# Kernel optimization log

Measured on AMD Instinct MI355X. Metric: run time of the kernel, lower is better.

The kernel has to match this reference:

```python
import jax, jax.numpy as jnp
import numpy as np
import math

H = 16  # heads
EPS_NORM = 1e-12
EPS_W = 1e-6


def setup_inputs() -> dict:
    key = jax.random.key(0)
    ks = jax.random.split(key, 6)
    B, T, d = 2, 2048, 1024
    s = 1.0 / math.sqrt(d)
    return {
        "x": jax.random.normal(ks[0], (B, T, d), dtype=jnp.float32),
        "Wq": jax.random.normal(ks[1], (d, d), dtype=jnp.float32) * s,
        "Wk": jax.random.normal(ks[2], (d, d), dtype=jnp.float32) * s,
        "Wv": jax.random.normal(ks[3], (d, d), dtype=jnp.float32) * s,
        "Wo": jax.random.normal(ks[4], (d, d), dtype=jnp.float32) * s,
        "bo": jnp.zeros((d,), dtype=jnp.float32),
    }


def _l2norm(t):
    # F.normalize(dim=-1): x / max(||x||, eps)
    n = jnp.sqrt(jnp.sum(t * t, axis=-1, keepdims=True))
    return t / jnp.maximum(n, EPS_NORM)


def reference(x, Wq, Wk, Wv, Wo, bo):
    B, T, d = x.shape
    dk = d // H
    # projections (torch Linear: y = x @ W.T), split heads -> [B, H, T, dk]
    def proj(W):
        return (x @ W.T).reshape(B, T, H, dk).transpose(0, 2, 1, 3)
    Q = _l2norm(proj(Wq))
    K = _l2norm(proj(Wk))
    V = proj(Wv)
    # angular similarity scores [B, H, T, T]
    sim = jnp.clip(jnp.einsum("bhqd,bhkd->bhqk", Q, K), -0.999, 0.999)
    scores = 1.0 - jnp.arccos(sim) / jnp.float32(math.pi)
    W = jnp.maximum(scores, EPS_W) ** 8
    W = W / (jnp.sum(W, axis=-1, keepdims=True) + EPS_W)
    out = jnp.einsum("bhqk,bhkd->bhqd", W, V)  # [B, H, T, dk]
    out = out.transpose(0, 2, 1, 3).reshape(B, T, d)
    return out @ Wo.T + bo
```

## Files before the change

### kernel.cpp

```cpp
#include <hip/hip_runtime.h>
#include <hip/hip_bf16.h>
#include <hip/hip_fp16.h>
#include <math.h>

#define BB 2
#define TT 2048
#define DD 1024
#define HH 16
#define DK 64
#define KT 64

typedef _Float16 f16x8 __attribute__((ext_vector_type(8)));
typedef __fp16 fp16x2 __attribute__((ext_vector_type(2)));
typedef __attribute__((ext_vector_type(4))) float f32x4;
typedef __attribute__((ext_vector_type(2))) float f32x2;

static __device__ __forceinline__ void g2lds16(const void* g, void* l) {
    __builtin_amdgcn_global_load_lds(
        (const __attribute__((address_space(1))) unsigned int*)g,
        (__attribute__((address_space(3))) unsigned int*)l, 16, 0, 0);
}

static __device__ __forceinline__ f32x2 w8pair(f32x2 s, f32x2& rs) {
    f32x2 ax;
    ax.x = fminf(fabsf(s.x), 0.999f);
    ax.y = fminf(fabsf(s.y), 0.999f);
    f32x2 p = ax * -0.0059617f + 0.0236380f;
    p = p * ax + (-0.0675180f);
    p = p * ax + 0.49997851f;
    f32x2 om = 1.0f - ax;
    f32x2 u;
    u.x = __builtin_amdgcn_sqrtf(om.x);
    u.y = __builtin_amdgcn_sqrtf(om.y);
    f32x2 uq = u * p;
    f32x2 e = 0.5f - uq;
    f32x2 t;
    t.x = 0.5f + copysignf(e.x, s.x);
    t.y = 0.5f + copysignf(e.y, s.y);
    f32x2 t2 = t * t;
    f32x2 t4 = t2 * t2;
    f32x2 t8 = t4 * t4;
    rs += t8;
    return t8;
}
static __device__ __forceinline__ int packh2(f32x2 v) {
    union { fp16x2 h; int i; } u;
    u.h = __builtin_amdgcn_cvt_pkrtz(v.x, v.y);
    return u.i;
}

__global__ __launch_bounds__(256) void cvtall_kernel(
    const float* __restrict__ x,  const float* __restrict__ Wq,
    const float* __restrict__ Wk, const float* __restrict__ Wv,
    const float* __restrict__ Wo,
    _Float16* __restrict__ xh, _Float16* __restrict__ W3h,
    _Float16* __restrict__ Woh)
{
    const int bid = blockIdx.x;
    const float* s; _Float16* d; int blk;
    if (bid < 2048) { s = x; d = xh; blk = bid; }
    else {
        const int idx = bid - 2048;
        const int w   = idx >> 9;
        blk = idx & 511;
        s = (w == 0) ? Wq : (w == 1) ? Wk : (w == 2) ? Wv : Wo;
        d = (w == 3) ? Woh : W3h + (size_t)w * (DD * DD);
    }
    const int i = (blk * 256 + threadIdx.x) * 8;
    float4 a = *(const float4*)(s + i);
    float4 b = *(const float4*)(s + i + 4);
    union { _Float16 h[8]; int4 v; } u;
    u.h[0] = (_Float16)a.x; u.h[1] = (_Float16)a.y;
    u.h[2] = (_Float16)a.z; u.h[3] = (_Float16)a.w;
    u.h[4] = (_Float16)b.x; u.h[5] = (_Float16)b.y;
    u.h[6] = (_Float16)b.z; u.h[7] = (_Float16)b.w;
    *(int4*)(d + i) = u.v;
}

__global__ __launch_bounds__(256, 3) void gemm_qkv(
    const _Float16* __restrict__ Ah_g, const _Float16* __restrict__ B_g,
    _Float16* __restrict__ Qh, _Float16* __restrict__ Kh,
    _Float16* __restrict__ Vh, int nbx, int K)
{
    __shared__ _Float16 Ahs[8][128][8];
    __shared__ _Float16 Bhs[8][128][8];

    const int nwg  = gridDim.x;
    const int wgid = blockIdx.x;
    const int cpx  = nwg >> 3;
    const int swz  = (wgid & 7) * cpx + (wgid >> 3);
    const int by   = swz / nbx;
    const int bx   = swz - by * nbx;

    const int t    = threadIdx.x;
    const int m0   = by * 128;
    const int n0g  = bx * 128;
    const int seg  = n0g >> 10;
    const int n0   = n0g & 1023;

    const int lane = t & 63;
    const int w    = t >> 6;
    const int wm   = w >> 1;
    const int wn   = w & 1;
    const int l15  = lane & 15;
    const int quad = lane >> 4;

    f32x4 acc[4][4];
#pragma unroll
    for (int i = 0; i < 4; ++i)
#pragma unroll
        for (int j = 0; j < 4; ++j) acc[i][j] = (f32x4)0.f;

    for (int k0 = 0; k0 < K; k0 += 64) {
        __syncthreads();
#pragma unroll
        for (int i = 0; i < 2; ++i) {
            const int cc = w * 2 + i;
#pragma unroll
            for (int half = 0; half < 2; ++half) {
                g2lds16(Ah_g + (size_t)(m0 + half * 64 + lane) * K + k0 + cc * 8,
                        &Ahs[cc][half * 64][0]);
                g2lds16(B_g + (size_t)(n0g + half * 64 + lane) * K + k0 + cc * 8,
                        &Bhs[cc][half * 64][0]);
            }
        }
        __syncthreads();

#pragma unroll
        for (int kh = 0; kh < 2; ++kh) {
            f16x8 ah[4], bh[4];
#pragma unroll
            for (int tm = 0; tm < 4; ++tm)
                ah[tm] = *(const f16x8*)&Ahs[kh * 4 + quad][wm * 64 + tm * 16 + l15][0];
#pragma unroll
            for (int tn = 0; tn < 4; ++tn)
                bh[tn] = *(const f16x8*)&Bhs[kh * 4 + quad][wn * 64 + tn * 16 + l15][0];
#pragma unroll
            for (int tm = 0; tm < 4; ++tm)
#pragma unroll
                for (int tn = 0; tn < 4; ++tn)
                    acc[tm][tn] = __builtin_amdgcn_mfma_f32_16x16x32_f16(
                        ah[tm], bh[tn], acc[tm][tn], 0, 0, 0);
        }
    }

    if (seg < 2) {
        _Float16* __restrict__ dstb = (seg == 0) ? Qh : Kh;
        const int hh = (n0 >> 6) + wn;
#pragma unroll
        for (int tm = 0; tm < 4; ++tm) {
#pragma unroll
            for (int r = 0; r < 4; ++r) {
                float ss = 0.f;
#pragma unroll
                for (int tn = 0; tn < 4; ++tn) {
                    const float v = acc[tm][tn][r];
                    ss += v * v;
                }
                ss += __shfl_xor(ss, 1);
                ss += __shfl_xor(ss, 2);
                ss += __shfl_xor(ss, 4);
                ss += __shfl_xor(ss, 8);
                const float inv = __builtin_amdgcn_rsqf(fmaxf(ss, 1e-24f));
                const int row = m0 + wm * 64 + tm * 16 + quad * 4 + r;
                const int b   = row >> 11;
                const int tt  = row & 2047;
                _Float16* dst = dstb + ((size_t)(b * HH + hh) * TT + tt) * DK;
#pragma unroll
                for (int tn = 0; tn < 4; ++tn)
                    dst[tn * 16 + l15] = (_Float16)(acc[tm][tn][r] * inv);
            }
        }
    } else {
#pragma unroll
        for (int tm = 0; tm < 4; ++tm)
#pragma unroll
            for (int tn = 0; tn < 4; ++tn) {
                const int col  = n0 + wn * 64 + tn * 16 + l15;
                const int rowb = m0 + wm * 64 + tm * 16 + quad * 4;
#pragma unroll
                for (int r = 0; r < 4; ++r)
                    Vh[(size_t)(rowb + r) * 1024 + col] =
                        (_Float16)acc[tm][tn][r];
            }
    }
}

__global__ __launch_bounds__(256) void gemm_wo(
    const _Float16* __restrict__ Ah_g, const _Float16* __restrict__ Al_g,
    const _Float16* __restrict__ B_g, const float* __restrict__ bias,
    float* __restrict__ C, int nbx, int K)
{
    __shared__ _Float16 Ahs[2][8][128][8];
    __shared__ _Float16 Als[2][8][128][8];
    __shared__ _Float16 Bhs[2][8][128][8];

    const int nwg  = gridDim.x;
    const int wgid = blockIdx.x;
    const int cpx  = nwg >> 3;
    const int swz  = (wgid & 7) * cpx + (wgid >> 3);
    const int by   = swz / nbx;
    const int bx   = swz - by * nbx;

    const int t    = threadIdx.x;
    const int m0   = by * 128;
    const int n0g  = bx * 128;

    const int lane = t & 63;
    const int w    = t >> 6;
    const int wm   = w >> 1;
    const int wn   = w & 1;
    const int l15  = lane & 15;
    const int quad = lane >> 4;

    f32x4 acc[4][4];
#pragma unroll
    for (int i = 0; i < 4; ++i)
#pragma unroll
        for (int j = 0; j < 4; ++j) acc[i][j] = (f32x4)0.f;

    auto STAGE = [&](int bf, int k0) {
#pragma unroll
        for (int i = 0; i < 2; ++i) {
            const int cc = w * 2 + i;
#pragma unroll
            for (int half = 0; half < 2; ++half) {
                g2lds16(Ah_g + (size_t)(m0 + half * 64 + lane) * K + k0 + cc * 8,
                        &Ahs[bf][cc][half * 64][0]);
                g2lds16(Al_g + (size_t)(m0 + half * 64 + lane) * K + k0 + cc * 8,
                        &Als[bf][cc][half * 64][0]);
                g2lds16(B_g + (size_t)(n0g + half * 64 + lane) * K + k0 + cc * 8,
                        &Bhs[bf][cc][half * 64][0]);
            }
        }
    };

    STAGE(0, 0);
    int cur = 0;
    for (int k0 = 0; k0 < K; k0 += 64) {
        __syncthreads();
        if (k0 + 64 < K) STAGE(cur ^ 1, k0 + 64);

#pragma unroll
        for (int kh = 0; kh < 2; ++kh) {
            f16x8 ah[4], al[4], bh[4];
#pragma unroll
            for (int tm = 0; tm < 4; ++tm) {
                ah[tm] = *(const f16x8*)&Ahs[cur][kh * 4 + quad][wm * 64 + tm * 16 + l15][0];
                al[tm] = *(const f16x8*)&Als[cur][kh * 4 + quad][wm * 64 + tm * 16 + l15][0];
            }
#pragma unroll
            for (int tn = 0; tn < 4; ++tn)
                bh[tn] = *(const f16x8*)&Bhs[cur][kh * 4 + quad][wn * 64 + tn * 16 + l15][0];
#pragma unroll
            for (int tm = 0; tm < 4; ++tm)
#pragma unroll
                for (int tn = 0; tn < 4; ++tn)
                    acc[tm][tn] = __builtin_amdgcn_mfma_f32_16x16x32_f16(
                        ah[tm], bh[tn], acc[tm][tn], 0, 0, 0);
#pragma unroll
            for (int tm = 0; tm < 4; ++tm)
#pragma unroll
                for (int tn = 0; tn < 4; ++tn)
                    acc[tm][tn] = __builtin_amdgcn_mfma_f32_16x16x32_f16(
                        al[tm], bh[tn], acc[tm][tn], 0, 0, 0);
        }
        cur ^= 1;
    }

#pragma unroll
    for (int tm = 0; tm < 4; ++tm)
#pragma unroll
        for (int tn = 0; tn < 4; ++tn) {
            const int col  = n0g + wn * 64 + tn * 16 + l15;
            const float bv = bias[col];
            const int rowb = m0 + wm * 64 + tm * 16 + quad * 4;
#pragma unroll
            for (int r = 0; r < 4; ++r)
                C[(size_t)(rowb + r) * 1024 + col] = acc[tm][tn][r] + bv;
        }
}

__global__ __launch_bounds__(256) void vtrans_kernel(
    const _Float16* __restrict__ Vh, _Float16* __restrict__ Vt)
{
    __shared__ _Float16 Vtmp[64][72];
    const int t  = threadIdx.x;
    const int t0 = blockIdx.x * 64;
    const int h  = blockIdx.y;
    const int b  = blockIdx.z;
    const int bh = b * HH + h;

    {
        const int i  = t >> 2;
        const int jc = (t & 3) * 16;
        const _Float16* src = Vh + (size_t)(b * TT + t0 + i) * DD + h * DK + jc;
        f16x8 a = *(const f16x8*)(src);
        f16x8 c = *(const f16x8*)(src + 8);
#pragma unroll
        for (int e = 0; e < 8; ++e) {
            Vtmp[jc + e][i]     = a[e];
            Vtmp[jc + 8 + e][i] = c[e];
        }
    }
    __syncthreads();
    {
        const int d  = t >> 2;
        const int kc = (t & 3) * 16;
        const int tc = (t0 + kc) >> 3;
        _Float16* dst = Vt + ((size_t)bh * (TT >> 3) + tc) * (64 * 8) + d * 8;
        *(int4*)(dst)          = *(const int4*)&Vtmp[d][kc];
        *(int4*)(dst + 64 * 8) = *(const int4*)&Vtmp[d][kc + 8];
    }
}

__global__ __launch_bounds__(256, 4) void attn_kernel(
    const _Float16* __restrict__ Qh_g, const _Float16* __restrict__ Kh_g,
    const _Float16* __restrict__ Vt_g,
    _Float16* __restrict__ Oh, _Float16* __restrict__ Ol)
{
    __shared__ _Float16 Vts[2][8][64][8];
    __shared__ _Float16 Ws[2][64][72];
    __shared__ float Rbuf[4][64];
    __shared__ float Rfin[64];

    const int t    = threadIdx.x;
    const int lane = t & 63;
    const int w    = t >> 6;
    const int l15  = lane & 15;
    const int quad = lane >> 4;
    const int q0   = blockIdx.x * 64;
    const int h    = blockIdx.y;
    const int b    = blockIdx.z;
    const size_t bh = (size_t)(b * HH + h);

    const _Float16* kh_g = Kh_g + bh * TT * DK;
    const _Float16* vt_g = Vt_g + bh * (size_t)(TT >> 3) * (64 * 8);

    f16x8 qf[4][2];
#pragma unroll
    for (int qt = 0; qt < 4; ++qt)
#pragma unroll
        for (int s = 0; s < 2; ++s)
            qf[qt][s] = *(const f16x8*)(Qh_g + (bh * TT + q0 + qt * 16 + l15) * DK
                                        + s * 32 + quad * 8);

    f16x8 kf[2], kfn[2];
#pragma unroll
    for (int s = 0; s < 2; ++s) {
        kf[s] = *(const f16x8*)(kh_g
            + (size_t)(w * 16 + l15) * DK + s * 32 + quad * 8);
        kfn[s] = kf[s];
    }

#pragma unroll
    for (int j = 0; j < 2; ++j) {
        const int kc = w * 2 + j;
        g2lds16(vt_g + (size_t)kc * (64 * 8) + lane * 8, &Vts[0][kc][0][0]);
    }

    f32x4 acc[4];
#pragma unroll
    for (int j = 0; j < 4; ++j) acc[j] = (f32x4)0.f;
    f32x2 rs2[4];
#pragma unroll
    for (int j = 0; j < 4; ++j) rs2[j] = (f32x2)0.f;

    int p = 0;
    for (int k0 = 0; k0 < TT; k0 += KT, p ^= 1) {
        const int kn = k0 + KT;
        if (kn < TT) {
#pragma unroll
            for (int s = 0; s < 2; ++s)
                kfn[s] = *(const f16x8*)(kh_g
                    + (size_t)(kn + w * 16 + l15) * DK + s * 32 + quad * 8);
        }

#pragma unroll
        for (int qt = 0; qt < 4; ++qt) {
            f32x4 c_ = (f32x4)0.f;
#pragma unroll
            for (int s = 0; s < 2; ++s)
                c_ = __builtin_amdgcn_mfma_f32_16x16x32_f16(
                    kf[s], qf[qt][s], c_, 0, 0, 0);
            f32x2 p01, p23;
            p01.x = c_[0]; p01.y = c_[1];
            p23.x = c_[2]; p23.y = c_[3];
            f32x2 w01 = w8pair(p01, rs2[qt]);
            f32x2 w23 = w8pair(p23, rs2[qt]);
            int2 pk;
            pk.x = packh2(w01);
            pk.y = packh2(w23);
            *(int2*)&Ws[p][qt * 16 + l15][w * 16 + quad * 4] = pk;
        }
        __syncthreads();

        if (kn < TT) {
#pragma unroll
            for (int j = 0; j < 2; ++j) {
                const int kc = w * 2 + j;
                g2lds16(vt_g + ((size_t)(kn >> 3) + kc) * (64 * 8) + lane * 8,
                        &Vts[p ^ 1][kc][0][0]);
            }
        }

#pragma unroll
        for (int kstep = 0; kstep < 2; ++kstep) {
            f16x8 av = *(const f16x8*)&Ws[p][16 * w + l15][kstep * 32 + quad * 8];
#pragma unroll
            for (int nd = 0; nd < 4; ++nd) {
                f16x8 bv = *(const f16x8*)&Vts[p][kstep * 4 + quad][nd * 16 + l15][0];
                acc[nd] = __builtin_amdgcn_mfma_f32_16x16x32_f16(
                    av, bv, acc[nd], 0, 0, 0);
            }
        }

#pragma unroll
        for (int s = 0; s < 2; ++s)
            kf[s] = kfn[s];
    }

#pragma unroll
    for (int qt = 0; qt < 4; ++qt) {
        float pr = rs2[qt].x + rs2[qt].y;
        pr += __shfl_xor(pr, 16);
        pr += __shfl_xor(pr, 32);
        if (quad == 0) Rbuf[w][qt * 16 + l15] = pr;
    }
    __syncthreads();
    if (t < 64) {
        float s = Rbuf[0][t] + Rbuf[1][t] + Rbuf[2][t] + Rbuf[3][t];
        Rfin[t] = 1.f / (s + 1e-6f);
    }
    __syncthreads();

#pragma unroll
    for (int r = 0; r < 4; ++r) {
        const int q = 16 * w + quad * 4 + r;
        const float inv = Rfin[q];
        const size_t base = (size_t)(b * TT + q0 + q) * DD + h * DK + l15;
#pragma unroll
        for (int nd = 0; nd < 4; ++nd) {
            float v = acc[nd][r] * inv;
            _Float16 hv = (_Float16)v;
            Oh[base + nd * 16] = hv;
            Ol[base + nd * 16] = (_Float16)(v - (float)hv);
        }
    }
}

extern "C" void kernel_launch(void* const* d_in, const int* in_sizes, int n_in,
                              void* d_out, int out_size, void* d_ws, size_t ws_size,
                              hipStream_t stream)
{
    const float* x  = (const float*)d_in[0];
    const float* Wq = (const float*)d_in[1];
    const float* Wk = (const float*)d_in[2];
    const float* Wv = (const float*)d_in[3];
    const float* Wo = (const float*)d_in[4];
    const float* bo = (const float*)d_in[5];
    float* out = (float*)d_out;

    const int M = BB * TT;

    const size_t MB = 1024 * 1024;
    char* ws = (char*)d_ws;
    _Float16* xh  = (_Float16*)(ws);
    _Float16* W3h = (_Float16*)(ws + 8 * MB);
    _Float16* Woh = (_Float16*)(ws + 14 * MB);
    _Float16* Qh  = (_Float16*)(ws + 16 * MB);
    _Float16* Kh  = (_Float16*)(ws + 24 * MB);
    _Float16* Vh  = (_Float16*)(ws + 32 * MB);
    _Float16* Vt  = (_Float16*)(ws + 40 * MB);
    _Float16* Oh  = (_Float16*)(ws);
    _Float16* Ol  = (_Float16*)(ws + 32 * MB);

    dim3 gB(256);

    cvtall_kernel<<<4096, gB, 0, stream>>>(x, Wq, Wk, Wv, Wo, xh, W3h, Woh);

    {
        const int nbx = 3072 / 128;
        const int nby = M / 128;
        gemm_qkv<<<nbx * nby, gB, 0, stream>>>(
            xh, W3h, Qh, Kh, Vh, nbx, DD);
    }

    vtrans_kernel<<<dim3(TT / 64, HH, BB), gB, 0, stream>>>(Vh, Vt);

    attn_kernel<<<dim3(TT / 64, HH, BB), gB, 0, stream>>>(Qh, Kh, Vt, Oh, Ol);

    {
        const int nbx = 1024 / 128;
        const int nby = M / 128;
        gemm_wo<<<nbx * nby, gB, 0, stream>>>(
            Oh, Ol, Woh, bo, out, nbx, DD);
    }
}
```

Before: 262.9 us.

## Fuse V transpose into QKV GEMM epilogue and retile XCD block mapping

The QKV GEMM epilogue now writes V directly in the blocked transposed layout the attention kernel reads, so the separate vtrans kernel and its round trip through global memory go away. Both GEMMs also replace the generic swizzle with a hardcoded mapping that gives each XCD a contiguous 2D block of output tiles, aiming for better L2 reuse. The V stores are now 8-byte scattered writes with a stride of 16 bytes between lanes, which may coalesce worse than the old row-major stores. Grid sizes are now hardcoded.

Result: no change. 258.5 us (-1.7%).

```diff
diff --git a/kernel.cpp b/kernel.cpp
--- a/kernel.cpp
+++ b/kernel.cpp
@@ -80,17 +80,16 @@
 __global__ __launch_bounds__(256, 3) void gemm_qkv(
     const _Float16* __restrict__ Ah_g, const _Float16* __restrict__ B_g,
     _Float16* __restrict__ Qh, _Float16* __restrict__ Kh,
-    _Float16* __restrict__ Vh, int nbx, int K)
+    _Float16* __restrict__ Vt, int K)
 {
     __shared__ _Float16 Ahs[8][128][8];
     __shared__ _Float16 Bhs[8][128][8];
 
-    const int nwg  = gridDim.x;
     const int wgid = blockIdx.x;
-    const int cpx  = nwg >> 3;
-    const int swz  = (wgid & 7) * cpx + (wgid >> 3);
-    const int by   = swz / nbx;
-    const int bx   = swz - by * nbx;
+    const int xcd  = wgid & 7;
+    const int idx  = wgid >> 3;
+    const int by   = (xcd >> 1) * 8  + idx / 12;
+    const int bx   = (xcd & 1) * 12 + idx % 12;
 
     const int t    = threadIdx.x;
     const int m0   = by * 128;
@@ -172,35 +171,44 @@
             }
         }
     } else {
-#pragma unroll
-        for (int tm = 0; tm < 4; ++tm)
+        const int hh = (n0 >> 6) + wn;
+#pragma unroll
+        for (int tm = 0; tm < 4; ++tm) {
+            const int row = m0 + wm * 64 + tm * 16 + quad * 4;
+            const int b   = row >> 11;
+            const int tt  = row & 2047;
+            const int c   = tt >> 3;
+            const int e   = tt & 7;
+            _Float16* dstc = Vt
+                + ((size_t)(b * HH + hh) * (TT >> 3) + c) * (64 * 8) + e;
 #pragma unroll
             for (int tn = 0; tn < 4; ++tn) {
-                const int col  = n0 + wn * 64 + tn * 16 + l15;
-                const int rowb = m0 + wm * 64 + tm * 16 + quad * 4;
-#pragma unroll
-                for (int r = 0; r < 4; ++r)
-                    Vh[(size_t)(rowb + r) * 1024 + col] =
-                        (_Float16)acc[tm][tn][r];
-            }
+                const int d = tn * 16 + l15;
+                union { _Float16 h[4]; int2 v; } uu;
+                uu.h[0] = (_Float16)acc[tm][tn][0];
+                uu.h[1] = (_Float16)acc[tm][tn][1];
+                uu.h[2] = (_Float16)acc[tm][tn][2];
+                uu.h[3] = (_Float16)acc[tm][tn][3];
+                *(int2*)(dstc + d * 8) = uu.v;
+            }
+        }
     }
 }
 
 __global__ __launch_bounds__(256) void gemm_wo(
     const _Float16* __restrict__ Ah_g, const _Float16* __restrict__ Al_g,
     const _Float16* __restrict__ B_g, const float* __restrict__ bias,
-    float* __restrict__ C, int nbx, int K)
+    float* __restrict__ C, int K)
 {
     __shared__ _Float16 Ahs[2][8][128][8];
     __shared__ _Float16 Als[2][8][128][8];
     __shared__ _Float16 Bhs[2][8][128][8];
 
-    const int nwg  = gridDim.x;
     const int wgid = blockIdx.x;
-    const int cpx  = nwg >> 3;
-    const int swz  = (wgid & 7) * cpx + (wgid >> 3);
-    const int by   = swz / nbx;
-    const int bx   = swz - by * nbx;
+    const int xcd  = wgid & 7;
+    const int idx  = wgid >> 3;
+    const int by   = (xcd >> 1) * 8 + idx / 4;
+    const int bx   = (xcd & 1) * 4 + idx % 4;
 
     const int t    = threadIdx.x;
     const int m0   = by * 128;
@@ -279,39 +287,6 @@
             for (int r = 0; r < 4; ++r)
                 C[(size_t)(rowb + r) * 1024 + col] = acc[tm][tn][r] + bv;
         }
-}
-
-__global__ __launch_bounds__(256) void vtrans_kernel(
-    const _Float16* __restrict__ Vh, _Float16* __restrict__ Vt)
-{
-    __shared__ _Float16 Vtmp[64][72];
-    const int t  = threadIdx.x;
-    const int t0 = blockIdx.x * 64;
-    const int h  = blockIdx.y;
-    const int b  = blockIdx.z;
-    const int bh = b * HH + h;
-
-    {
-        const int i  = t >> 2;
-        const int jc = (t & 3) * 16;
-        const _Float16* src = Vh + (size_t)(b * TT + t0 + i) * DD + h * DK + jc;
-        f16x8 a = *(const f16x8*)(src);
-        f16x8 c = *(const f16x8*)(src + 8);
-#pragma unroll
-        for (int e = 0; e < 8; ++e) {
-            Vtmp[jc + e][i]     = a[e];
-            Vtmp[jc + 8 + e][i] = c[e];
-        }
-    }
-    __syncthreads();
-    {
-        const int d  = t >> 2;
-        const int kc = (t & 3) * 16;
-        const int tc = (t0 + kc) >> 3;
-        _Float16* dst = Vt + ((size_t)bh * (TT >> 3) + tc) * (64 * 8) + d * 8;
-        *(int4*)(dst)          = *(const int4*)&Vtmp[d][kc];
-        *(int4*)(dst + 64 * 8) = *(const int4*)&Vtmp[d][kc + 8];
-    }
 }
 
 __global__ __launch_bounds__(256, 4) void attn_kernel(
@@ -461,8 +436,6 @@
     const float* bo = (const float*)d_in[5];
     float* out = (float*)d_out;
 
-    const int M = BB * TT;
-
     const size_t MB = 1024 * 1024;
     char* ws = (char*)d_ws;
     _Float16* xh  = (_Float16*)(ws);
@@ -470,30 +443,17 @@
     _Float16* Woh = (_Float16*)(ws + 14 * MB);
     _Float16* Qh  = (_Float16*)(ws + 16 * MB);
     _Float16* Kh  = (_Float16*)(ws + 24 * MB);
-    _Float16* Vh  = (_Float16*)(ws + 32 * MB);
+    _Float16* Ol  = (_Float16*)(ws + 32 * MB);
     _Float16* Vt  = (_Float16*)(ws + 40 * MB);
     _Float16* Oh  = (_Float16*)(ws);
-    _Float16* Ol  = (_Float16*)(ws + 32 * MB);
 
     dim3 gB(256);
 
     cvtall_kernel<<<4096, gB, 0, stream>>>(x, Wq, Wk, Wv, Wo, xh, W3h, Woh);
 
-    {
-        const int nbx = 3072 / 128;
-        const int nby = M / 128;
-        gemm_qkv<<<nbx * nby, gB, 0, stream>>>(
-            xh, W3h, Qh, Kh, Vh, nbx, DD);
-    }
-
-    vtrans_kernel<<<dim3(TT / 64, HH, BB), gB, 0, stream>>>(Vh, Vt);
+    gemm_qkv<<<768, gB, 0, stream>>>(xh, W3h, Qh, Kh, Vt, DD);
 
     attn_kernel<<<dim3(TT / 64, HH, BB), gB, 0, stream>>>(Qh, Kh, Vt, Oh, Ol);
 
-    {
-        const int nbx = 1024 / 128;
-        const int nby = M / 128;
-        gemm_wo<<<nbx * nby, gB, 0, stream>>>(
-            Oh, Ol, Woh, bo, out, nbx, DD);
-    }
-}
+    gemm_wo<<<256, gB, 0, stream>>>(Oh, Ol, Woh, bo, out, DD);
+}
```
